# Kernel optimization log

Hardware: AMD Instinct MI355X
Metric: run time of the kernel (lower is better)

The kernel has to match this reference:

```python
import jax, jax.numpy as jnp
import numpy as np

B, S, D, H = 8192, 45, 64, 8
HD = D // H          # head_dim = 8
FF = 4 * D           # FFN inner dim = 256


def _layernorm(x, g, b, eps=1e-5):
    m = x.mean(-1, keepdims=True)
    v = ((x - m) ** 2).mean(-1, keepdims=True)
    return (x - m) * jax.lax.rsqrt(v + eps) * g + b


def setup_inputs() -> dict:
    key = jax.random.key(0)
    ks = jax.random.split(key, 8)
    s = 1.0 / np.sqrt(D)
    sf = 1.0 / np.sqrt(FF)
    return {
        "x": jax.random.normal(ks[0], (B, S, D), jnp.float32),
        "Wq": jax.random.normal(ks[1], (D, D), jnp.float32) * s,
        "bq": jnp.zeros((D,), jnp.float32),
        "Wk": jax.random.normal(ks[2], (D, D), jnp.float32) * s,
        "bk": jnp.zeros((D,), jnp.float32),
        "Wv": jax.random.normal(ks[3], (D, D), jnp.float32) * s,
        "bv": jnp.zeros((D,), jnp.float32),
        "Wo": jax.random.normal(ks[4], (D, D), jnp.float32) * s,
        "bo": jnp.zeros((D,), jnp.float32),
        "ln1_g": jnp.ones((D,), jnp.float32),
        "ln1_b": jnp.zeros((D,), jnp.float32),
        "W1": jax.random.normal(ks[5], (D, FF), jnp.float32) * s,
        "b1": jnp.zeros((FF,), jnp.float32),
        "W2": jax.random.normal(ks[6], (FF, D), jnp.float32) * sf,
        "b2": jnp.zeros((D,), jnp.float32),
        "ln2_g": jnp.ones((D,), jnp.float32),
        "ln2_b": jnp.zeros((D,), jnp.float32),
    }


def reference(x, Wq, bq, Wk, bk, Wv, bv, Wo, bo, ln1_g, ln1_b, W1, b1, W2, b2, ln2_g, ln2_b):
    b, s, d = x.shape
    # sinusoidal positional encoding (PositionalEncoding(hidden_dim, max_len=45))
    pos = jnp.arange(s, dtype=jnp.float32)[:, None]
    div = jnp.exp(-jnp.log(jnp.float32(10000.0)) * jnp.arange(0, d, 2, dtype=jnp.float32) / d)
    ang = pos * div                              # [S, D/2]
    pe = jnp.zeros((s, d), x.dtype).at[:, 0::2].set(jnp.sin(ang)).at[:, 1::2].set(jnp.cos(ang))
    h = x + pe                                   # [B, S, D]
    residual = h
    # torch.nn.MultiheadAttention, batch_first=True, 8 heads, head_dim 8
    q = (h @ Wq + bq).reshape(b, s, H, HD).transpose(0, 2, 1, 3)  # [B,H,S,HD]
    k = (h @ Wk + bk).reshape(b, s, H, HD).transpose(0, 2, 1, 3)
    v = (h @ Wv + bv).reshape(b, s, H, HD).transpose(0, 2, 1, 3)
    scores = jnp.einsum('bhqd,bhkd->bhqk', q, k) / jnp.sqrt(jnp.float32(HD))
    attn = jax.nn.softmax(scores, axis=-1)
    o = jnp.einsum('bhqk,bhkd->bhqd', attn, v).transpose(0, 2, 1, 3).reshape(b, s, d)
    o = o @ Wo + bo
    # norm(out + alpha * residual), alpha = 1
    h2 = _layernorm(o + residual, ln1_g, ln1_b)
    # FFN: Linear -> ReLU -> Linear, residual + LayerNorm (standard transformer FFN)
    f = jax.nn.relu(h2 @ W1 + b1) @ W2 + b2
    return _layernorm(h2 + f, ln2_g, ln2_b)
```

## Files before the change

kernel.cpp:

```cpp
#include <hip/hip_runtime.h>
#include <hip/hip_bf16.h>
#include <math.h>

#define NB 8192
#define S_ 45
#define D_ 64
#define FF_ 256
#define LDH 68
#define HBS 72
#define VTS 72
#define FBS 280

typedef __attribute__((ext_vector_type(4))) float f32x4;
typedef __attribute__((ext_vector_type(8))) short s16x8;
typedef __attribute__((ext_vector_type(4))) short s16x4;

#define WS_QKV 11520
#define WS_WO  36096
#define WS_W1  44288
#define WS_W2  77056

__device__ inline short f2bf(float f) {
    __hip_bfloat16 h = __float2bfloat16(f);
    return *reinterpret_cast<short*>(&h);
}
__device__ inline float bf2f(short s) {
    union { unsigned u; float f; } c;
    c.u = ((unsigned)(unsigned short)s) << 16;
    return c.f;
}

__global__ void prep_kernel(const float* __restrict__ Wq, const float* __restrict__ Wk,
                            const float* __restrict__ Wv, const float* __restrict__ Wo,
                            const float* __restrict__ W1, const float* __restrict__ W2,
                            void* __restrict__ ws) {
    float* pe   = (float*)ws;
    short* wqkv = (short*)((char*)ws + WS_QKV);
    short* wo   = (short*)((char*)ws + WS_WO);
    short* w1   = (short*)((char*)ws + WS_W1);
    short* w2   = (short*)((char*)ws + WS_W2);
    int i = blockIdx.x * 256 + threadIdx.x;
    if (i < S_ * D_) {
        int s = i / D_, d = i % D_;
        float div = expf(-logf(10000.0f) * (float)(d & ~1) / (float)D_);
        float ang = (float)s * div;
        pe[i] = (d & 1) ? cosf(ang) : sinf(ang);
    }
    if (i < 12288) {
        int n = i >> 6, k = i & 63;
        const float* W = (n < 64) ? Wq : (n < 128 ? Wk : Wv);
        wqkv[i] = f2bf(W[k * 64 + (n & 63)]);
    }
    if (i < 4096) {
        int n = i >> 6, k = i & 63;
        wo[i] = f2bf(Wo[k * 64 + n]);
    }
    if (i < 16384) {
        int n = i >> 6, k = i & 63;
        w1[i] = f2bf(W1[k * FF_ + n]);
        int n2 = i >> 8, k2 = i & 255;
        w2[i] = f2bf(W2[k2 * 64 + n2]);
    }
}

__launch_bounds__(512, 1)
__global__ void encoder_kernel(
    const float* __restrict__ x,
    const float* __restrict__ bq, const float* __restrict__ bk,
    const float* __restrict__ bv, const float* __restrict__ bo,
    const float* __restrict__ ln1g, const float* __restrict__ ln1b,
    const float* __restrict__ b1, const float* __restrict__ b2,
    const float* __restrict__ ln2g, const float* __restrict__ ln2b,
    const void* __restrict__ ws,
    float* __restrict__ out)
{
    const float* pe    = (const float*)ws;
    const short* wqkvT = (const short*)((const char*)ws + WS_QKV);
    const short* woT   = (const short*)((const char*)ws + WS_WO);
    const short* w1T   = (const short*)((const char*)ws + WS_W1);
    const short* w2T   = (const short*)((const char*)ws + WS_W2);

    __shared__ __align__(16) char pool[38016];
    short* hb = (short*)pool;
    short* qb = (short*)(pool + 6912);
    short* kb = (short*)(pool + 13824);
    short* vT = (short*)(pool + 20736);
    short* ob = (short*)(pool + 31104);
    float* t1 = (float*)(pool + 6912);
    short* fb = (short*)(pool + 6912);
    float* t2 = (float*)(pool + 6912);

    const int t = threadIdx.x;
    const int b = blockIdx.x;
    const int w = t >> 6, l = t & 63;
    const int lr = l & 15, lg = l >> 4;
    const s16x8 zero8 = {0, 0, 0, 0, 0, 0, 0, 0};

    {
        const float4* x4 = (const float4*)(x + (size_t)b * (S_ * D_));
        const float4* p4 = (const float4*)pe;
        for (int i = t; i < S_ * D_ / 4; i += 512) {
            int r = i >> 4, c4 = (i & 15) << 2;
            float4 a = x4[i], p = p4[i];
            s16x4 hv16 = { f2bf(a.x + p.x), f2bf(a.y + p.y),
                           f2bf(a.z + p.z), f2bf(a.w + p.w) };
            *(s16x4*)&hb[r * HBS + c4] = hv16;
        }
        for (int i = t; i < 3 * HBS; i += 512) hb[45 * HBS + i] = 0;
    }
    __syncthreads();

    {
        const float SC2 = 0.35355339059327373f * 1.44269504088896340f;
        for (int id = w; id < 36; id += 8) {
            const int m0 = (id % 3) << 4, n0 = (id / 3) << 4;
            f32x4 acc = {0.f, 0.f, 0.f, 0.f};
            #pragma unroll
            for (int k0 = 0; k0 < 64; k0 += 32) {
                s16x8 af = *(const s16x8*)&hb[(m0 + lr) * HBS + k0 + lg * 8];
                s16x8 bf = *(const s16x8*)&wqkvT[(n0 + lr) * 64 + k0 + lg * 8];
                acc = __builtin_amdgcn_mfma_f32_16x16x32_bf16(af, bf, acc, 0, 0, 0);
            }
            if (n0 < 64) {
                const float bias = bq[n0 + lr];
                #pragma unroll
                for (int r = 0; r < 4; ++r)
                    qb[(m0 + lg * 4 + r) * HBS + n0 + lr] = f2bf((acc[r] + bias) * SC2);
            } else if (n0 < 128) {
                const int cc = n0 - 64 + lr;
                const float bias = bk[cc];
                #pragma unroll
                for (int r = 0; r < 4; ++r)
                    kb[(m0 + lg * 4 + r) * HBS + cc] = f2bf(acc[r] + bias);
            } else {
                const int cc = n0 - 128 + lr;
                const float bias = bv[cc];
                s16x4 vv = { f2bf(acc[0] + bias), f2bf(acc[1] + bias),
                             f2bf(acc[2] + bias), f2bf(acc[3] + bias) };
                *(s16x4*)&vT[cc * VTS + m0 + lg * 4] = vv;
            }
        }
    }
    __syncthreads();

    {
        const int hd = w << 3;
        s16x8 pv_b0 = *(const s16x8*)&vT[(hd + lr) * VTS + lg * 8];
        s16x8 pv_b1 = (lg < 2) ? *(const s16x8*)&vT[(hd + lr) * VTS + 32 + lg * 8]
                               : zero8;
        s16x8 kaf[3];
        #pragma unroll
        for (int tm = 0; tm < 3; ++tm)
            kaf[tm] = (lg == 0) ? *(const s16x8*)&kb[(tm * 16 + lr) * HBS + hd] : zero8;
        #pragma unroll
        for (int tn = 0; tn < 3; ++tn) {
            s16x8 qbf = (lg == 0) ? *(const s16x8*)&qb[(tn * 16 + lr) * HBS + hd] : zero8;
            f32x4 S[3];
            #pragma unroll
            for (int tm = 0; tm < 3; ++tm) {
                f32x4 z = {0.f, 0.f, 0.f, 0.f};
                S[tm] = __builtin_amdgcn_mfma_f32_16x16x32_bf16(kaf[tm], qbf, z, 0, 0, 0);
            }
            float psum = 0.f;
            #pragma unroll
            for (int tm = 0; tm < 3; ++tm) {
                #pragma unroll
                for (int r = 0; r < 4; ++r) {
                    float e = __builtin_amdgcn_exp2f(S[tm][r]);
                    if (tm == 2) e = (lg * 4 + r >= 13) ? 0.f : e;
                    S[tm][r] = e;
                    psum += e;
                }
            }
            float s = psum;
            s += __shfl_xor(s, 16);
            s += __shfl_xor(s, 32);
            float inv = 1.0f / s;
            unsigned pk0[3], pk1[3];
            #pragma unroll
            for (int tm = 0; tm < 3; ++tm) {
                float a0 = S[tm][0] * inv, a1 = S[tm][1] * inv;
                float a2 = S[tm][2] * inv, a3 = S[tm][3] * inv;
                pk0[tm] = (__float_as_uint(a0) >> 16) | (__float_as_uint(a1) & 0xFFFF0000u);
                pk1[tm] = (__float_as_uint(a2) >> 16) | (__float_as_uint(a3) & 0xFFFF0000u);
            }
            const int srcA = lr + ((lg & 1) << 5);
            const int srcB = srcA + 16;
            unsigned gA0[3], gA1[3], gB0[3], gB1[3];
            #pragma unroll
            for (int tm = 0; tm < 3; ++tm) {
                gA0[tm] = (unsigned)__shfl((int)pk0[tm], srcA);
                gA1[tm] = (unsigned)__shfl((int)pk1[tm], srcA);
                gB0[tm] = (unsigned)__shfl((int)pk0[tm], srcB);
                gB1[tm] = (unsigned)__shfl((int)pk1[tm], srcB);
            }
            const bool tm1 = (lg >> 1) != 0;
            union { unsigned u[4]; s16x8 v; } a1c, a2c;
            a1c.u[0] = tm1 ? gA0[1] : gA0[0];
            a1c.u[1] = tm1 ? gA1[1] : gA1[0];
            a1c.u[2] = tm1 ? gB0[1] : gB0[0];
            a1c.u[3] = tm1 ? gB1[1] : gB1[0];
            const bool lo = (lg < 2);
            a2c.u[0] = lo ? gA0[2] : 0u;
            a2c.u[1] = lo ? gA1[2] : 0u;
            a2c.u[2] = lo ? gB0[2] : 0u;
            a2c.u[3] = lo ? gB1[2] : 0u;
            f32x4 z = {0.f, 0.f, 0.f, 0.f};
            f32x4 O = __builtin_amdgcn_mfma_f32_16x16x32_bf16(a1c.v, pv_b0, z, 0, 0, 0);
            O = __builtin_amdgcn_mfma_f32_16x16x32_bf16(a2c.v, pv_b1, O, 0, 0, 0);
            if (lr < 8) {
                #pragma unroll
                for (int r = 0; r < 4; ++r) {
                    int row = tn * 16 + lg * 4 + r;
                    if (row < S_) ob[row * HBS + hd + lr] = f2bf(O[r]);
                }
            }
        }
    }
    __syncthreads();

    {
        for (int id = w; id < 12; id += 8) {
            const int m0 = (id % 3) << 4, n0 = (id / 3) << 4;
            f32x4 acc = {0.f, 0.f, 0.f, 0.f};
            #pragma unroll
            for (int k0 = 0; k0 < 64; k0 += 32) {
                s16x8 af = *(const s16x8*)&ob[(m0 + lr) * HBS + k0 + lg * 8];
                s16x8 bf = *(const s16x8*)&woT[(n0 + lr) * 64 + k0 + lg * 8];
                acc = __builtin_amdgcn_mfma_f32_16x16x32_bf16(af, bf, acc, 0, 0, 0);
            }
            const int col = n0 + lr;
            const float bias = bo[col];
            #pragma unroll
            for (int r = 0; r < 4; ++r) {
                int row = m0 + lg * 4 + r;
                if (row < S_)
                    t1[row * LDH + col] = acc[r] + bias + bf2f(hb[row * HBS + col]);
            }
        }
    }
    __syncthreads();

    {
        if (t < S_ * 8) {
            const int row = t >> 3, d0 = (t & 7) << 3;
            float4 v1 = *(const float4*)&t1[row * LDH + d0];
            float4 v2 = *(const float4*)&t1[row * LDH + d0 + 4];
            float s  = v1.x + v1.y + v1.z + v1.w + v2.x + v2.y + v2.z + v2.w;
            float s2 = v1.x*v1.x + v1.y*v1.y + v1.z*v1.z + v1.w*v1.w +
                       v2.x*v2.x + v2.y*v2.y + v2.z*v2.z + v2.w*v2.w;
            s  += __shfl_xor(s, 1);  s  += __shfl_xor(s, 2);  s  += __shfl_xor(s, 4);
            s2 += __shfl_xor(s2, 1); s2 += __shfl_xor(s2, 2); s2 += __shfl_xor(s2, 4);
            float mean = s * (1.0f / 64.0f);
            float var  = s2 * (1.0f / 64.0f) - mean * mean;
            float rstd = rsqrtf(var + 1e-5f);
            float4 g1 = *(const float4*)&ln1g[d0], g2 = *(const float4*)&ln1g[d0 + 4];
            float4 b1v = *(const float4*)&ln1b[d0], b2v = *(const float4*)&ln1b[d0 + 4];
            s16x8 o16;
            o16[0] = f2bf((v1.x - mean) * rstd * g1.x + b1v.x);
            o16[1] = f2bf((v1.y - mean) * rstd * g1.y + b1v.y);
            o16[2] = f2bf((v1.z - mean) * rstd * g1.z + b1v.z);
            o16[3] = f2bf((v1.w - mean) * rstd * g1.w + b1v.w);
            o16[4] = f2bf((v2.x - mean) * rstd * g2.x + b2v.x);
            o16[5] = f2bf((v2.y - mean) * rstd * g2.y + b2v.y);
            o16[6] = f2bf((v2.z - mean) * rstd * g2.z + b2v.z);
            o16[7] = f2bf((v2.w - mean) * rstd * g2.w + b2v.w);
            *(s16x8*)&hb[row * HBS + d0] = o16;
        }
    }
    __syncthreads();

    {
        for (int id = w; id < 48; id += 8) {
            const int m0 = (id % 3) << 4, nl = (id / 3) << 4;
            f32x4 acc = {0.f, 0.f, 0.f, 0.f};
            #pragma unroll
            for (int k0 = 0; k0 < 64; k0 += 32) {
                s16x8 af = *(const s16x8*)&hb[(m0 + lr) * HBS + k0 + lg * 8];
                s16x8 bf = *(const s16x8*)&w1T[(nl + lr) * 64 + k0 + lg * 8];
                acc = __builtin_amdgcn_mfma_f32_16x16x32_bf16(af, bf, acc, 0, 0, 0);
            }
            const float bias = b1[nl + lr];
            #pragma unroll
            for (int r = 0; r < 4; ++r) {
                int row = m0 + lg * 4 + r;
                if (row < S_)
                    fb[row * FBS + nl + lr] = f2bf(fmaxf(acc[r] + bias, 0.f));
            }
        }
    }
    __syncthreads();

    f32x4 facc0 = {0.f, 0.f, 0.f, 0.f};
    f32x4 facc1 = {0.f, 0.f, 0.f, 0.f};
    {
        const int m0 = (w % 3) << 4, n0 = (w / 3) << 4;
        #pragma unroll 4
        for (int k0 = 0; k0 < FF_; k0 += 32) {
            s16x8 af = *(const s16x8*)&fb[(m0 + lr) * FBS + k0 + lg * 8];
            s16x8 bf = *(const s16x8*)&w2T[(n0 + lr) * 256 + k0 + lg * 8];
            facc0 = __builtin_amdgcn_mfma_f32_16x16x32_bf16(af, bf, facc0, 0, 0, 0);
        }
        if (w < 4) {
            const int id = w + 8;
            const int m1 = (id % 3) << 4, n1 = (id / 3) << 4;
            #pragma unroll 4
            for (int k0 = 0; k0 < FF_; k0 += 32) {
                s16x8 af = *(const s16x8*)&fb[(m1 + lr) * FBS + k0 + lg * 8];
                s16x8 bf = *(const s16x8*)&w2T[(n1 + lr) * 256 + k0 + lg * 8];
                facc1 = __builtin_amdgcn_mfma_f32_16x16x32_bf16(af, bf, facc1, 0, 0, 0);
            }
        }
    }
    __syncthreads();
    {
        const int m0 = (w % 3) << 4, n0 = (w / 3) << 4;
        const int col = n0 + lr;
        const float bias = b2[col];
        #pragma unroll
        for (int r = 0; r < 4; ++r) {
            int row = m0 + lg * 4 + r;
            if (row < S_)
                t2[row * LDH + col] = facc0[r] + bias + bf2f(hb[row * HBS + col]);
        }
        if (w < 4) {
            const int id = w + 8;
            const int m1 = (id % 3) << 4, n1 = (id / 3) << 4;
            const int col1 = n1 + lr;
            const float bias1 = b2[col1];
            #pragma unroll
            for (int r = 0; r < 4; ++r) {
                int row = m1 + lg * 4 + r;
                if (row < S_)
                    t2[row * LDH + col1] = facc1[r] + bias1 + bf2f(hb[row * HBS + col1]);
            }
        }
    }
    __syncthreads();

    {
        if (t < S_ * 8) {
            const int row = t >> 3, d0 = (t & 7) << 3;
            float4 v1 = *(const float4*)&t2[row * LDH + d0];
            float4 v2 = *(const float4*)&t2[row * LDH + d0 + 4];
            float s  = v1.x + v1.y + v1.z + v1.w + v2.x + v2.y + v2.z + v2.w;
            float s2 = v1.x*v1.x + v1.y*v1.y + v1.z*v1.z + v1.w*v1.w +
                       v2.x*v2.x + v2.y*v2.y + v2.z*v2.z + v2.w*v2.w;
            s  += __shfl_xor(s, 1);  s  += __shfl_xor(s, 2);  s  += __shfl_xor(s, 4);
            s2 += __shfl_xor(s2, 1); s2 += __shfl_xor(s2, 2); s2 += __shfl_xor(s2, 4);
            float mean = s * (1.0f / 64.0f);
            float var  = s2 * (1.0f / 64.0f) - mean * mean;
            float rstd = rsqrtf(var + 1e-5f);
            float4 g1 = *(const float4*)&ln2g[d0], g2 = *(const float4*)&ln2g[d0 + 4];
            float4 b1v = *(const float4*)&ln2b[d0], b2v = *(const float4*)&ln2b[d0 + 4];
            float4 o1, o2;
            o1.x = (v1.x - mean) * rstd * g1.x + b1v.x;
            o1.y = (v1.y - mean) * rstd * g1.y + b1v.y;
            o1.z = (v1.z - mean) * rstd * g1.z + b1v.z;
            o1.w = (v1.w - mean) * rstd * g1.w + b1v.w;
            o2.x = (v2.x - mean) * rstd * g2.x + b2v.x;
            o2.y = (v2.y - mean) * rstd * g2.y + b2v.y;
            o2.z = (v2.z - mean) * rstd * g2.z + b2v.z;
            o2.w = (v2.w - mean) * rstd * g2.w + b2v.w;
            float* op = out + (size_t)b * (S_ * D_) + row * 64 + d0;
            *(float4*)op = o1;
            *(float4*)(op + 4) = o2;
        }
    }
}

extern "C" void kernel_launch(void* const* d_in, const int* in_sizes, int n_in,
                              void* d_out, int out_size, void* d_ws, size_t ws_size,
                              hipStream_t stream) {
    const float* x    = (const float*)d_in[0];
    const float* Wq   = (const float*)d_in[1];
    const float* bq   = (const float*)d_in[2];
    const float* Wk   = (const float*)d_in[3];
    const float* bk   = (const float*)d_in[4];
    const float* Wv   = (const float*)d_in[5];
    const float* bv   = (const float*)d_in[6];
    const float* Wo   = (const float*)d_in[7];
    const float* bo   = (const float*)d_in[8];
    const float* ln1g = (const float*)d_in[9];
    const float* ln1b = (const float*)d_in[10];
    const float* W1   = (const float*)d_in[11];
    const float* b1   = (const float*)d_in[12];
    const float* W2   = (const float*)d_in[13];
    const float* b2   = (const float*)d_in[14];
    const float* ln2g = (const float*)d_in[15];
    const float* ln2b = (const float*)d_in[16];
    float* out = (float*)d_out;

    hipLaunchKernelGGL(prep_kernel, dim3(64), dim3(256), 0, stream,
                       Wq, Wk, Wv, Wo, W1, W2, d_ws);
    hipLaunchKernelGGL(encoder_kernel, dim3(NB), dim3(512), 0, stream,
                       x, bq, bk, bv, bo, ln1g, ln1b, b1, b2, ln2g, ln2b,
                       d_ws, out);
}
```

Measured before the change: 299.1 us.

## Process two batch elements per block with four waves each

```diff
diff --git a/kernel.cpp b/kernel.cpp
--- a/kernel.cpp
+++ b/kernel.cpp
@@ -10,6 +10,7 @@
 #define HBS 72
 #define VTS 72
 #define FBS 280
+#define EPB 38016
 
 typedef __attribute__((ext_vector_type(4))) float f32x4;
 typedef __attribute__((ext_vector_type(8))) short s16x8;
@@ -80,39 +81,45 @@
     const short* w1T   = (const short*)((const char*)ws + WS_W1);
     const short* w2T   = (const short*)((const char*)ws + WS_W2);
 
-    __shared__ __align__(16) char pool[38016];
-    short* hb = (short*)pool;
-    short* qb = (short*)(pool + 6912);
-    short* kb = (short*)(pool + 13824);
-    short* vT = (short*)(pool + 20736);
-    short* ob = (short*)(pool + 31104);
-    float* t1 = (float*)(pool + 6912);
-    short* fb = (short*)(pool + 6912);
-    float* t2 = (float*)(pool + 6912);
+    __shared__ __align__(16) char pool[2 * EPB];
 
     const int t = threadIdx.x;
-    const int b = blockIdx.x;
     const int w = t >> 6, l = t & 63;
     const int lr = l & 15, lg = l >> 4;
+    const int elem = w >> 2;
+    const int we   = w & 3;
+    const int te   = t & 255;
+    const size_t e = (size_t)blockIdx.x * 2 + elem;
+
+    char* ep = pool + elem * EPB;
+    short* hb = (short*)ep;
+    short* qb = (short*)(ep + 6912);
+    short* kb = (short*)(ep + 13824);
+    short* vT = (short*)(ep + 20736);
+    short* ob = (short*)(ep + 31104);
+    float* t1 = (float*)(ep + 6912);
+    short* fb = (short*)(ep + 6912);
+    float* t2 = (float*)(ep + 6912);
+
     const s16x8 zero8 = {0, 0, 0, 0, 0, 0, 0, 0};
 
     {
-        const float4* x4 = (const float4*)(x + (size_t)b * (S_ * D_));
+        const float4* x4 = (const float4*)(x + e * (S_ * D_));
         const float4* p4 = (const float4*)pe;
-        for (int i = t; i < S_ * D_ / 4; i += 512) {
+        for (int i = te; i < S_ * D_ / 4; i += 256) {
             int r = i >> 4, c4 = (i & 15) << 2;
             float4 a = x4[i], p = p4[i];
             s16x4 hv16 = { f2bf(a.x + p.x), f2bf(a.y + p.y),
                            f2bf(a.z + p.z), f2bf(a.w + p.w) };
             *(s16x4*)&hb[r * HBS + c4] = hv16;
         }
-        for (int i = t; i < 3 * HBS; i += 512) hb[45 * HBS + i] = 0;
+        for (int i = te; i < 3 * HBS; i += 256) hb[45 * HBS + i] = 0;
     }
     __syncthreads();
 
     {
         const float SC2 = 0.35355339059327373f * 1.44269504088896340f;
-        for (int id = w; id < 36; id += 8) {
+        for (int id = we; id < 36; id += 4) {
             const int m0 = (id % 3) << 4, n0 = (id / 3) << 4;
             f32x4 acc = {0.f, 0.f, 0.f, 0.f};
             #pragma unroll
@@ -144,83 +151,85 @@
     __syncthreads();
 
     {
-        const int hd = w << 3;
-        s16x8 pv_b0 = *(const s16x8*)&vT[(hd + lr) * VTS + lg * 8];
-        s16x8 pv_b1 = (lg < 2) ? *(const s16x8*)&vT[(hd + lr) * VTS + 32 + lg * 8]
-                               : zero8;
-        s16x8 kaf[3];
-        #pragma unroll
-        for (int tm = 0; tm < 3; ++tm)
-            kaf[tm] = (lg == 0) ? *(const s16x8*)&kb[(tm * 16 + lr) * HBS + hd] : zero8;
-        #pragma unroll
-        for (int tn = 0; tn < 3; ++tn) {
-            s16x8 qbf = (lg == 0) ? *(const s16x8*)&qb[(tn * 16 + lr) * HBS + hd] : zero8;
-            f32x4 S[3];
-            #pragma unroll
-            for (int tm = 0; tm < 3; ++tm) {
+        for (int hh = 0; hh < 2; ++hh) {
+            const int hd = (we + (hh << 2)) << 3;
+            s16x8 pv_b0 = *(const s16x8*)&vT[(hd + lr) * VTS + lg * 8];
+            s16x8 pv_b1 = (lg < 2) ? *(const s16x8*)&vT[(hd + lr) * VTS + 32 + lg * 8]
+                                   : zero8;
+            s16x8 kaf[3];
+            #pragma unroll
+            for (int tm = 0; tm < 3; ++tm)
+                kaf[tm] = (lg == 0) ? *(const s16x8*)&kb[(tm * 16 + lr) * HBS + hd] : zero8;
+            #pragma unroll
+            for (int tn = 0; tn < 3; ++tn) {
+                s16x8 qbf = (lg == 0) ? *(const s16x8*)&qb[(tn * 16 + lr) * HBS + hd] : zero8;
+                f32x4 S[3];
+                #pragma unroll
+                for (int tm = 0; tm < 3; ++tm) {
+                    f32x4 z = {0.f, 0.f, 0.f, 0.f};
+                    S[tm] = __builtin_amdgcn_mfma_f32_16x16x32_bf16(kaf[tm], qbf, z, 0, 0, 0);
+                }
+                float psum = 0.f;
+                #pragma unroll
+                for (int tm = 0; tm < 3; ++tm) {
+                    #pragma unroll
+                    for (int r = 0; r < 4; ++r) {
+                        float e2 = __builtin_amdgcn_exp2f(S[tm][r]);
+                        if (tm == 2) e2 = (lg * 4 + r >= 13) ? 0.f : e2;
+                        S[tm][r] = e2;
+                        psum += e2;
+                    }
+                }
+                float s = psum;
+                s += __shfl_xor(s, 16);
+                s += __shfl_xor(s, 32);
+                float inv = 1.0f / s;
+                unsigned pk0[3], pk1[3];
+                #pragma unroll
+                for (int tm = 0; tm < 3; ++tm) {
+                    float a0 = S[tm][0] * inv, a1 = S[tm][1] * inv;
+                    float a2 = S[tm][2] * inv, a3 = S[tm][3] * inv;
+                    pk0[tm] = (__float_as_uint(a0) >> 16) | (__float_as_uint(a1) & 0xFFFF0000u);
+                    pk1[tm] = (__float_as_uint(a2) >> 16) | (__float_as_uint(a3) & 0xFFFF0000u);
+                }
+                const int srcA = lr + ((lg & 1) << 5);
+                const int srcB = srcA + 16;
+                unsigned gA0[3], gA1[3], gB0[3], gB1[3];
+                #pragma unroll
+                for (int tm = 0; tm < 3; ++tm) {
+                    gA0[tm] = (unsigned)__shfl((int)pk0[tm], srcA);
+                    gA1[tm] = (unsigned)__shfl((int)pk1[tm], srcA);
+                    gB0[tm] = (unsigned)__shfl((int)pk0[tm], srcB);
+                    gB1[tm] = (unsigned)__shfl((int)pk1[tm], srcB);
+                }
+                const bool tm1 = (lg >> 1) != 0;
+                union { unsigned u[4]; s16x8 v; } a1c, a2c;
+                a1c.u[0] = tm1 ? gA0[1] : gA0[0];
+                a1c.u[1] = tm1 ? gA1[1] : gA1[0];
+                a1c.u[2] = tm1 ? gB0[1] : gB0[0];
+                a1c.u[3] = tm1 ? gB1[1] : gB1[0];
+                const bool lo = (lg < 2);
+                a2c.u[0] = lo ? gA0[2] : 0u;
+                a2c.u[1] = lo ? gA1[2] : 0u;
+                a2c.u[2] = lo ? gB0[2] : 0u;
+                a2c.u[3] = lo ? gB1[2] : 0u;
                 f32x4 z = {0.f, 0.f, 0.f, 0.f};
-                S[tm] = __builtin_amdgcn_mfma_f32_16x16x32_bf16(kaf[tm], qbf, z, 0, 0, 0);
-            }
-            float psum = 0.f;
-            #pragma unroll
-            for (int tm = 0; tm < 3; ++tm) {
-                #pragma unroll
-                for (int r = 0; r < 4; ++r) {
-                    float e = __builtin_amdgcn_exp2f(S[tm][r]);
-                    if (tm == 2) e = (lg * 4 + r >= 13) ? 0.f : e;
-                    S[tm][r] = e;
-                    psum += e;
+                f32x4 O = __builtin_amdgcn_mfma_f32_16x16x32_bf16(a1c.v, pv_b0, z, 0, 0, 0);
+                O = __builtin_amdgcn_mfma_f32_16x16x32_bf16(a2c.v, pv_b1, O, 0, 0, 0);
+                if (lr < 8) {
+                    #pragma unroll
+                    for (int r = 0; r < 4; ++r) {
+                        int row = tn * 16 + lg * 4 + r;
+                        if (row < S_) ob[row * HBS + hd + lr] = f2bf(O[r]);
+                    }
                 }
             }
-            float s = psum;
-            s += __shfl_xor(s, 16);
-            s += __shfl_xor(s, 32);
-            float inv = 1.0f / s;
-            unsigned pk0[3], pk1[3];
-            #pragma unroll
-            for (int tm = 0; tm < 3; ++tm) {
-                float a0 = S[tm][0] * inv, a1 = S[tm][1] * inv;
-                float a2 = S[tm][2] * inv, a3 = S[tm][3] * inv;
-                pk0[tm] = (__float_as_uint(a0) >> 16) | (__float_as_uint(a1) & 0xFFFF0000u);
-                pk1[tm] = (__float_as_uint(a2) >> 16) | (__float_as_uint(a3) & 0xFFFF0000u);
-            }
-            const int srcA = lr + ((lg & 1) << 5);
-            const int srcB = srcA + 16;
-            unsigned gA0[3], gA1[3], gB0[3], gB1[3];
-            #pragma unroll
-            for (int tm = 0; tm < 3; ++tm) {
-                gA0[tm] = (unsigned)__shfl((int)pk0[tm], srcA);
-                gA1[tm] = (unsigned)__shfl((int)pk1[tm], srcA);
-                gB0[tm] = (unsigned)__shfl((int)pk0[tm], srcB);
-                gB1[tm] = (unsigned)__shfl((int)pk1[tm], srcB);
-            }
-            const bool tm1 = (lg >> 1) != 0;
-            union { unsigned u[4]; s16x8 v; } a1c, a2c;
-            a1c.u[0] = tm1 ? gA0[1] : gA0[0];
-            a1c.u[1] = tm1 ? gA1[1] : gA1[0];
-            a1c.u[2] = tm1 ? gB0[1] : gB0[0];
-            a1c.u[3] = tm1 ? gB1[1] : gB1[0];
-            const bool lo = (lg < 2);
-            a2c.u[0] = lo ? gA0[2] : 0u;
-            a2c.u[1] = lo ? gA1[2] : 0u;
-            a2c.u[2] = lo ? gB0[2] : 0u;
-            a2c.u[3] = lo ? gB1[2] : 0u;
-            f32x4 z = {0.f, 0.f, 0.f, 0.f};
-            f32x4 O = __builtin_amdgcn_mfma_f32_16x16x32_bf16(a1c.v, pv_b0, z, 0, 0, 0);
-            O = __builtin_amdgcn_mfma_f32_16x16x32_bf16(a2c.v, pv_b1, O, 0, 0, 0);
-            if (lr < 8) {
-                #pragma unroll
-                for (int r = 0; r < 4; ++r) {
-                    int row = tn * 16 + lg * 4 + r;
-                    if (row < S_) ob[row * HBS + hd + lr] = f2bf(O[r]);
-                }
-            }
-        }
-    }
-    __syncthreads();
-
-    {
-        for (int id = w; id < 12; id += 8) {
+        }
+    }
+    __syncthreads();
+
+    {
+        for (int id = we; id < 12; id += 4) {
             const int m0 = (id % 3) << 4, n0 = (id / 3) << 4;
             f32x4 acc = {0.f, 0.f, 0.f, 0.f};
             #pragma unroll
@@ -242,8 +251,8 @@
     __syncthreads();
 
     {
-        if (t < S_ * 8) {
-            const int row = t >> 3, d0 = (t & 7) << 3;
+        for (int slot = te; slot < S_ * 8; slot += 256) {
+            const int row = slot >> 3, d0 = (slot & 7) << 3;
             float4 v1 = *(const float4*)&t1[row * LDH + d0];
             float4 v2 = *(const float4*)&t1[row * LDH + d0 + 4];
             float s  = v1.x + v1.y + v1.z + v1.w + v2.x + v2.y + v2.z + v2.w;
@@ -271,7 +280,7 @@
     __syncthreads();
 
     {
-        for (int id = w; id < 48; id += 8) {
+        for (int id = we; id < 48; id += 4) {
             const int m0 = (id % 3) << 4, nl = (id / 3) << 4;
             f32x4 acc = {0.f, 0.f, 0.f, 0.f};
             #pragma unroll
@@ -291,56 +300,61 @@
     }
     __syncthreads();
 
-    f32x4 facc0 = {0.f, 0.f, 0.f, 0.f};
-    f32x4 facc1 = {0.f, 0.f, 0.f, 0.f};
-    {
-        const int m0 = (w % 3) << 4, n0 = (w / 3) << 4;
-        #pragma unroll 4
-        for (int k0 = 0; k0 < FF_; k0 += 32) {
-            s16x8 af = *(const s16x8*)&fb[(m0 + lr) * FBS + k0 + lg * 8];
-            s16x8 bf = *(const s16x8*)&w2T[(n0 + lr) * 256 + k0 + lg * 8];
-            facc0 = __builtin_amdgcn_mfma_f32_16x16x32_bf16(af, bf, facc0, 0, 0, 0);
-        }
-        if (w < 4) {
-            const int id = w + 8;
-            const int m1 = (id % 3) << 4, n1 = (id / 3) << 4;
+    f32x4 fa0 = {0.f, 0.f, 0.f, 0.f};
+    f32x4 fa1 = {0.f, 0.f, 0.f, 0.f};
+    f32x4 fa2 = {0.f, 0.f, 0.f, 0.f};
+    {
+        const int i0 = we, i1 = we + 4, i2 = we + 8;
+        {
+            const int m0 = (i0 % 3) << 4, n0 = (i0 / 3) << 4;
             #pragma unroll 4
             for (int k0 = 0; k0 < FF_; k0 += 32) {
-                s16x8 af = *(const s16x8*)&fb[(m1 + lr) * FBS + k0 + lg * 8];
-                s16x8 bf = *(const s16x8*)&w2T[(n1 + lr) * 256 + k0 + lg * 8];
-                facc1 = __builtin_amdgcn_mfma_f32_16x16x32_bf16(af, bf, facc1, 0, 0, 0);
-            }
-        }
-    }
-    __syncthreads();
-    {
-        const int m0 = (w % 3) << 4, n0 = (w / 3) << 4;
-        const int col = n0 + lr;
-        const float bias = b2[col];
-        #pragma unroll
-        for (int r = 0; r < 4; ++r) {
-            int row = m0 + lg * 4 + r;
-            if (row < S_)
-                t2[row * LDH + col] = facc0[r] + bias + bf2f(hb[row * HBS + col]);
-        }
-        if (w < 4) {
-            const int id = w + 8;
-            const int m1 = (id % 3) << 4, n1 = (id / 3) << 4;
-            const int col1 = n1 + lr;
-            const float bias1 = b2[col1];
+                s16x8 af = *(const s16x8*)&fb[(m0 + lr) * FBS + k0 + lg * 8];
+                s16x8 bf = *(const s16x8*)&w2T[(n0 + lr) * 256 + k0 + lg * 8];
+                fa0 = __builtin_amdgcn_mfma_f32_16x16x32_bf16(af, bf, fa0, 0, 0, 0);
+            }
+        }
+        {
+            const int m0 = (i1 % 3) << 4, n0 = (i1 / 3) << 4;
+            #pragma unroll 4
+            for (int k0 = 0; k0 < FF_; k0 += 32) {
+                s16x8 af = *(const s16x8*)&fb[(m0 + lr) * FBS + k0 + lg * 8];
+                s16x8 bf = *(const s16x8*)&w2T[(n0 + lr) * 256 + k0 + lg * 8];
+                fa1 = __builtin_amdgcn_mfma_f32_16x16x32_bf16(af, bf, fa1, 0, 0, 0);
+            }
+        }
+        {
+            const int m0 = (i2 % 3) << 4, n0 = (i2 / 3) << 4;
+            #pragma unroll 4
+            for (int k0 = 0; k0 < FF_; k0 += 32) {
+                s16x8 af = *(const s16x8*)&fb[(m0 + lr) * FBS + k0 + lg * 8];
+                s16x8 bf = *(const s16x8*)&w2T[(n0 + lr) * 256 + k0 + lg * 8];
+                fa2 = __builtin_amdgcn_mfma_f32_16x16x32_bf16(af, bf, fa2, 0, 0, 0);
+            }
+        }
+    }
+    __syncthreads();
+    {
+        auto t2_tile = [&](int id, const f32x4& fa) {
+            const int m0 = (id % 3) << 4, n0 = (id / 3) << 4;
+            const int col = n0 + lr;
+            const float bias = b2[col];
             #pragma unroll
             for (int r = 0; r < 4; ++r) {
-                int row = m1 + lg * 4 + r;
+                int row = m0 + lg * 4 + r;
                 if (row < S_)
-                    t2[row * LDH + col1] = facc1[r] + bias1 + bf2f(hb[row * HBS + col1]);
-            }
-        }
-    }
-    __syncthreads();
-
-    {
-        if (t < S_ * 8) {
-            const int row = t >> 3, d0 = (t & 7) << 3;
+                    t2[row * LDH + col] = fa[r] + bias + bf2f(hb[row * HBS + col]);
+            }
+        };
+        t2_tile(we, fa0);
+        t2_tile(we + 4, fa1);
+        t2_tile(we + 8, fa2);
+    }
+    __syncthreads();
+
+    {
+        for (int slot = te; slot < S_ * 8; slot += 256) {
+            const int row = slot >> 3, d0 = (slot & 7) << 3;
             float4 v1 = *(const float4*)&t2[row * LDH + d0];
             float4 v2 = *(const float4*)&t2[row * LDH + d0 + 4];
             float s  = v1.x + v1.y + v1.z + v1.w + v2.x + v2.y + v2.z + v2.w;
@@ -362,7 +376,7 @@
             o2.y = (v2.y - mean) * rstd * g2.y + b2v.y;
             o2.z = (v2.z - mean) * rstd * g2.z + b2v.z;
             o2.w = (v2.w - mean) * rstd * g2.w + b2v.w;
-            float* op = out + (size_t)b * (S_ * D_) + row * 64 + d0;
+            float* op = out + e * (S_ * D_) + row * 64 + d0;
             *(float4*)op = o1;
             *(float4*)(op + 4) = o2;
         }
@@ -393,7 +407,7 @@
 
     hipLaunchKernelGGL(prep_kernel, dim3(64), dim3(256), 0, stream,
                        Wq, Wk, Wv, Wo, W1, W2, d_ws);
-    hipLaunchKernelGGL(encoder_kernel, dim3(NB), dim3(512), 0, stream,
+    hipLaunchKernelGGL(encoder_kernel, dim3(NB / 2), dim3(512), 0, stream,
                        x, bq, bk, bv, bo, ln1g, ln1b, b1, b2, ln2g, ln2b,
                        d_ws, out);
 }
```

After: 316.7 us. 1.06x slower.
